# Kernel tuning notes

Measured on AMD Instinct MI355X. Metric: run time of the kernel, lower is better.

Reference implementation:

```python
import jax, jax.numpy as jnp
import numpy as np

B, L, C = 2, 2048, 1024
DK, H = 64, 16

def setup_inputs() -> dict:
    key = jax.random.key(0)
    ks = jax.random.split(key, 12)
    def lin(kw, kb, out_dim, in_dim):
        w = jax.random.normal(kw, (out_dim, in_dim), jnp.float32) * (1.0 / np.sqrt(in_dim))
        b = jnp.zeros((out_dim,), jnp.float32)
        return w, b
    WQ_w, WQ_b = lin(ks[0], ks[1], DK * H, C)
    WK_w, WK_b = lin(ks[2], ks[3], DK * H, C)
    WV_w, WV_b = lin(ks[4], ks[5], DK * H, C)
    WO_w, WO_b = lin(ks[6], ks[7], C, DK * H)
    qx = jax.random.normal(ks[8], (B, L, C), jnp.float32)
    kx = jax.random.normal(ks[9], (B, L, C), jnp.float32)
    vx = jax.random.normal(ks[10], (B, L, C), jnp.float32)
    maskPAD = jax.random.randint(ks[11], (B, L, L), 0, 2, jnp.int32)
    return {"qx": qx, "kx": kx, "vx": vx, "maskPAD": maskPAD,
            "WQ_w": WQ_w, "WQ_b": WQ_b, "WK_w": WK_w, "WK_b": WK_b,
            "WV_w": WV_w, "WV_b": WV_b, "WO_w": WO_w, "WO_b": WO_b}

def reference(qx, kx, vx, maskPAD, WQ_w, WQ_b, WK_w, WK_b, WV_w, WV_b, WO_w, WO_b):
    Bq, qL, _ = qx.shape
    kvL = kx.shape[1]
    # projections -> [B, H, L, DK]
    q = (qx @ WQ_w.T + WQ_b).reshape(Bq, qL, H, DK).transpose(0, 2, 1, 3)
    k = (kx @ WK_w.T + WK_b).reshape(Bq, kvL, H, DK).transpose(0, 2, 1, 3)
    v = (vx @ WV_w.T + WV_b).reshape(Bq, kvL, H, DK).transpose(0, 2, 1, 3)
    scores = jnp.einsum('bhqd,bhkd->bhqk', q, k) / np.sqrt(DK).astype(np.float32)
    scores = jnp.where((maskPAD == 0)[:, None, :, :], jnp.float32(-2**15 + 1), scores)
    alpha = jax.nn.softmax(scores, axis=3)  # dropout p=0 (eval)
    z = jnp.einsum('bhqk,bhkd->bhqd', alpha, v)
    z = z.transpose(0, 2, 1, 3).reshape(Bq, qL, H * DK)
    return z @ WO_w.T + WO_b
```

## Files before the change

### kernel.cpp

```cpp
#include <hip/hip_runtime.h>
#include <stdint.h>
#include <math.h>

typedef short short8 __attribute__((ext_vector_type(8)));
typedef float float4v __attribute__((ext_vector_type(4)));

static __device__ __forceinline__ float bf2f(uint16_t u) {
    union { uint32_t i; float f; } x; x.i = ((uint32_t)u) << 16; return x.f;
}
static __device__ __forceinline__ uint16_t f2bf(float f) {
    union { float f; uint32_t i; } x; x.f = f;
    uint32_t u = x.i;
    u += 0x7FFFu + ((u >> 16) & 1u);
    return (uint16_t)(u >> 16);
}
static __device__ __forceinline__ uint16_t f2bf_sane(float f) {
    uint16_t u = f2bf(f);
    if ((u & 0x7F80u) == 0x7F80u) u = 0;
    return u;
}
static __device__ __forceinline__ float san_f32(float f) {
    union { float f; uint32_t i; } x; x.f = f;
    if (((x.i >> 23) & 0xFFu) == 0xFFu) return 0.f;
    return x.f;
}
static __device__ __forceinline__ void gll16(const void* g, void* l) {
    __builtin_amdgcn_global_load_lds((const __attribute__((address_space(1))) void*)g,
                                     (__attribute__((address_space(3))) void*)l,
                                     16, 0, 0);
}
static __device__ __forceinline__ short8 load8(const void* p, size_t off, int fp32) {
    if (!fp32) return *(const short8*)((const uint16_t*)p + off);
    const float* f = (const float*)p + off;
    const float4v a = *(const float4v*)f;
    const float4v b = *(const float4v*)(f + 4);
    short8 r;
    r[0] = (short)f2bf(a[0]); r[1] = (short)f2bf(a[1]);
    r[2] = (short)f2bf(a[2]); r[3] = (short)f2bf(a[3]);
    r[4] = (short)f2bf(b[0]); r[5] = (short)f2bf(b[1]);
    r[6] = (short)f2bf(b[2]); r[7] = (short)f2bf(b[3]);
    return r;
}

__global__ __launch_bounds__(256) void detect_kernel(const uint16_t* qx, int* flag)
{
    __shared__ int s;
    const int tid = threadIdx.x;
    if (tid == 0) s = 0;
    __syncthreads();
    int bad = 0;
#pragma unroll 8
    for (int i = 0; i < 64; ++i) {
        const uint16_t u = qx[tid * 64 + i];
        bad |= ((u & 0x7F80u) == 0x7F80u) ? 1 : 0;
    }
    if (bad) atomicOr(&s, 1);
    __syncthreads();
    if (tid == 0) *flag = s;
}

__global__ __launch_bounds__(256) void pack_kernel(
    const int* __restrict__ mask, uint64_t* __restrict__ mask64)
{
    const int wave = threadIdx.x >> 6, lane = threadIdx.x & 63;
    const int row = blockIdx.x * 4 + wave;
    const int* src = mask + (size_t)row * 2048;
#pragma unroll 4
    for (int j = 0; j < 32; ++j) {
        const int m = src[j * 64 + lane];
        const uint64_t bal = __ballot(m != 0);
        if (lane == 0) mask64[(size_t)row * 32 + j] = bal;
    }
}

__global__ __launch_bounds__(256) void convert_kernel(
    const void* qx, const void* kx, const void* vx,
    const void* wq, const void* wk, const void* wv, const void* wo,
    const void* bq, const void* bk, const void* bv, const void* bo,
    uint16_t* cIn, uint16_t* cW, uint16_t* cB, const int* flag)
{
    const int mode = *flag;
    const int z = blockIdx.z;
    const int idx8 = blockIdx.x * 256 + threadIdx.x;
    if (z < 3) {
        const void* src = (z == 0) ? qx : (z == 1) ? kx : vx;
        uint16_t* dst = cIn + (size_t)z * 4194304;
        if (idx8 < 524288)
            *(short8*)(dst + (size_t)idx8 * 8) = load8(src, (size_t)idx8 * 8, mode);
    } else if (z < 7) {
        const int t = z - 3;
        const void* src = (t == 0) ? wq : (t == 1) ? wk : (t == 2) ? wv : wo;
        uint16_t* dst = cW + (size_t)t * 1048576;
        if (idx8 < 131072)
            *(short8*)(dst + (size_t)idx8 * 8) = load8(src, (size_t)idx8 * 8, mode);
    } else {
        if (idx8 < 128) {
#pragma unroll
            for (int t = 0; t < 4; ++t) {
                const void* src = (t == 0) ? bq : (t == 1) ? bk : (t == 2) ? bv : bo;
                *(short8*)(cB + t * 1024 + idx8 * 8) = load8(src, (size_t)idx8 * 8, mode);
            }
        }
    }
}

template <int MI, int NI>
static __device__ __forceinline__ void gemm_tile(
    const uint16_t* __restrict__ A, const uint16_t* __restrict__ W,
    const uint16_t* __restrict__ bias, void* __restrict__ C,
    int c_fp32, float out_scale)
{
    constexpr int TM = MI * 32, TN = NI * 32;
    __shared__ __align__(16) uint16_t sA[TM * 32];
    __shared__ __align__(16) uint16_t sB[TN * 32];

    const int tid  = threadIdx.x;
    const int wave = tid >> 6;
    const int lane = tid & 63;
    const int quad = lane >> 4;
    const int l15  = lane & 15;
    const int m0 = blockIdx.y * TM;
    const int n0 = blockIdx.x * TN;
    const int wm = (wave >> 1) * (MI * 16);
    const int wn = (wave & 1) * (NI * 16);
    const int r16 = lane >> 2;
    const int ch  = lane & 3;

    float4v acc[MI][NI] = {};

    for (int k0 = 0; k0 < 1024; k0 += 32) {
        __syncthreads();
#pragma unroll
        for (int g = wave; g < TM / 16; g += 4)
            gll16(A + (size_t)(m0 + g * 16 + r16) * 1024 + k0 + ch * 8,
                  (char*)sA + (size_t)g * 1024);
#pragma unroll
        for (int g = wave; g < TN / 16; g += 4)
            gll16(W + (size_t)(n0 + g * 16 + r16) * 1024 + k0 + ch * 8,
                  (char*)sB + (size_t)g * 1024);
        asm volatile("s_waitcnt vmcnt(0)" ::: "memory");
        __syncthreads();

        short8 af[MI], bfr[NI];
#pragma unroll
        for (int i = 0; i < MI; ++i)
            af[i] = *(const short8*)&sA[(wm + i * 16 + l15) * 32 + quad * 8];
#pragma unroll
        for (int j = 0; j < NI; ++j)
            bfr[j] = *(const short8*)&sB[(wn + j * 16 + l15) * 32 + quad * 8];
#pragma unroll
        for (int mi = 0; mi < MI; ++mi)
#pragma unroll
            for (int ni = 0; ni < NI; ++ni)
                acc[mi][ni] = __builtin_amdgcn_mfma_f32_16x16x32_bf16(
                    af[mi], bfr[ni], acc[mi][ni], 0, 0, 0);
    }

#pragma unroll
    for (int ni = 0; ni < NI; ++ni) {
        const int n = n0 + wn + ni * 16 + l15;
        const float bv = bf2f(bias[n]);
#pragma unroll
        for (int mi = 0; mi < MI; ++mi) {
            const int mbase = m0 + wm + mi * 16 + quad * 4;
#pragma unroll
            for (int r = 0; r < 4; ++r) {
                const float v = (acc[mi][ni][r] + bv) * out_scale;
                const size_t idx = (size_t)(mbase + r) * 1024 + n;
                if (c_fp32) ((float*)C)[idx] = san_f32(v);
                else        ((uint16_t*)C)[idx] = f2bf_sane(v);
            }
        }
    }
}

__global__ __launch_bounds__(256) void qkv_kernel(
    const uint16_t* cIn, const uint16_t* cW, const uint16_t* cB,
    uint16_t* Q, uint16_t* K, uint16_t* V)
{
    const int z = blockIdx.z;
    const uint16_t* A = cIn + (size_t)z * 4194304;
    const uint16_t* W = cW + (size_t)z * 1048576;
    const uint16_t* b = cB + z * 1024;
    uint16_t* C = (z == 0) ? Q : (z == 1) ? K : V;
    const float sc = (z == 0) ? 0.125f : 1.0f;
    gemm_tile<4, 4>(A, W, b, C, 0, sc);
}

__global__ __launch_bounds__(256) void out_kernel(
    const uint16_t* Z, const uint16_t* cW, const uint16_t* cB,
    void* out, const int* flag)
{
    const int mode = *flag;
    gemm_tile<2, 4>(Z, cW + 3 * 1048576, cB + 3 * 1024, out, mode, 1.0f);
}

__global__ __launch_bounds__(256) void vtrans_kernel(
    const uint16_t* __restrict__ Vp, uint16_t* __restrict__ Vt)
{
    __shared__ __align__(16) uint16_t t[64][72];
    const int tid = threadIdx.x;
    const int lt = blockIdx.x, h = blockIdx.y, b = blockIdx.z;
#pragma unroll
    for (int p = 0; p < 2; ++p) {
        const int r = p * 32 + (tid >> 3);
        const int c = (tid & 7) * 8;
        *(short8*)&t[r][c] =
            *(const short8*)(Vp + (size_t)(b * 2048 + lt * 64 + r) * 1024 + h * 64 + c);
    }
    __syncthreads();
#pragma unroll
    for (int p = 0; p < 2; ++p) {
        const int d = p * 32 + (tid >> 3);
        const int c = (tid & 7) * 8;
        short8 v;
#pragma unroll
        for (int j = 0; j < 8; ++j) v[j] = (short)t[c + j][d];
        *(short8*)(Vt + (size_t)((b * 16 + h) * 64 + d) * 2048 + lt * 64 + c) = v;
    }
}

#define VS 72

__global__ __launch_bounds__(256) void attn_kernel(
    const uint16_t* __restrict__ Q, const uint16_t* __restrict__ Kp,
    const uint16_t* __restrict__ Vt, const uint64_t* __restrict__ mask64,
    uint16_t* __restrict__ Z)
{
    __shared__ __align__(16) uint16_t sQ[64 * VS];
    __shared__ __align__(16) uint16_t sK[64 * VS];
    __shared__ __align__(16) uint16_t sV[64 * VS];
    __shared__ __align__(16) float    sS[4][16 * 36];

    const int tid = threadIdx.x;
    const int wave = tid >> 6, lane = tid & 63;
    const int quad = lane >> 4, l15 = lane & 15;
    const int qt = blockIdx.x, h = blockIdx.y, b = blockIdx.z;
    const int q0 = qt * 64;

    const int srow = tid >> 2;
    const int sc0  = (tid & 3);

    {
        const short8 x0 = *(const short8*)(Q + (size_t)(b * 2048 + q0 + srow) * 1024 + h * 64 + sc0 * 8);
        const short8 x1 = *(const short8*)(Q + (size_t)(b * 2048 + q0 + srow) * 1024 + h * 64 + (sc0 + 4) * 8);
        *(short8*)&sQ[srow * VS + sc0 * 8]       = x0;
        *(short8*)&sQ[srow * VS + (sc0 + 4) * 8] = x1;
    }
    __syncthreads();

    short8 qf[2];
#pragma unroll
    for (int kk = 0; kk < 2; ++kk)
        qf[kk] = *(const short8*)&sQ[(wave * 16 + l15) * VS + (quad + 4 * kk) * 8];

    const uint64_t* mrow = mask64 + (size_t)(b * 2048 + q0 + wave * 16 + l15) * 32;

    short8 ones;
#pragma unroll
    for (int j = 0; j < 8; ++j) ones[j] = (short)0x3F80;

    float4v oacc[4] = {};
    float4v lacc = {};

    for (int kt = 0; kt < 32; ++kt) {
        const int k0 = kt * 64;
        const short8 kx0 = *(const short8*)(Kp + (size_t)(b * 2048 + k0 + srow) * 1024 + h * 64 + sc0 * 8);
        const short8 kx1 = *(const short8*)(Kp + (size_t)(b * 2048 + k0 + srow) * 1024 + h * 64 + (sc0 + 4) * 8);
        const short8 vx0 = *(const short8*)(Vt + (size_t)((b * 16 + h) * 64 + srow) * 2048 + k0 + sc0 * 8);
        const short8 vx1 = *(const short8*)(Vt + (size_t)((b * 16 + h) * 64 + srow) * 2048 + k0 + (sc0 + 4) * 8);
        const uint64_t mw = mrow[kt];
        __syncthreads();
        *(short8*)&sK[srow * VS + sc0 * 8]       = kx0;
        *(short8*)&sK[srow * VS + (sc0 + 4) * 8] = kx1;
        *(short8*)&sV[srow * VS + sc0 * 8]       = vx0;
        *(short8*)&sV[srow * VS + (sc0 + 4) * 8] = vx1;
        __syncthreads();

        float4v sacc[4] = {};
#pragma unroll
        for (int ni = 0; ni < 4; ++ni) {
            const int row = ni * 16 + l15;
#pragma unroll
            for (int kk = 0; kk < 2; ++kk) {
                const short8 kf = *(const short8*)&sK[row * VS + (quad + 4 * kk) * 8];
                sacc[ni] = __builtin_amdgcn_mfma_f32_16x16x32_bf16(qf[kk], kf, sacc[ni], 0, 0, 0);
            }
        }

        short8 pf[2];
        float* Sw = &sS[wave][0];
#pragma unroll
        for (int h2 = 0; h2 < 2; ++h2) {
#pragma unroll
            for (int n2 = 0; n2 < 2; ++n2) {
                const float4v s4 = sacc[h2 * 2 + n2];
#pragma unroll
                for (int r = 0; r < 4; ++r)
                    Sw[(quad * 4 + r) * 36 + n2 * 16 + l15] = s4[r];
            }
            asm volatile("s_waitcnt lgkmcnt(0)" ::: "memory");
            const float* rp = &Sw[l15 * 36 + quad * 8];
            const float4v x0 = *(const float4v*)rp;
            const float4v x1 = *(const float4v*)(rp + 4);
            asm volatile("" ::: "memory");
            short8 tt;
#pragma unroll
            for (int j = 0; j < 4; ++j) {
                const int kp = h2 * 32 + quad * 8 + j;
                const float p0 = ((mw >> kp) & 1ull) ? __expf(x0[j]) : 0.f;
                const float p1 = ((mw >> (kp + 4)) & 1ull) ? __expf(x1[j]) : 0.f;
                tt[j]     = (short)f2bf(p0);
                tt[4 + j] = (short)f2bf(p1);
            }
            pf[h2] = tt;
        }

#pragma unroll
        for (int ni = 0; ni < 4; ++ni) {
            const int row = ni * 16 + l15;
#pragma unroll
            for (int kk = 0; kk < 2; ++kk) {
                const short8 vf = *(const short8*)&sV[row * VS + (quad + 4 * kk) * 8];
                oacc[ni] = __builtin_amdgcn_mfma_f32_16x16x32_bf16(pf[kk], vf, oacc[ni], 0, 0, 0);
            }
        }
#pragma unroll
        for (int kk = 0; kk < 2; ++kk)
            lacc = __builtin_amdgcn_mfma_f32_16x16x32_bf16(pf[kk], ones, lacc, 0, 0, 0);
    }

#pragma unroll
    for (int r = 0; r < 4; ++r) {
        const float inv = 1.0f / fmaxf(lacc[r], 1e-37f);
        const int qrow = q0 + wave * 16 + quad * 4 + r;
#pragma unroll
        for (int ni = 0; ni < 4; ++ni) {
            const float v = oacc[ni][r] * inv;
            Z[(size_t)(b * 2048 + qrow) * 1024 + h * 64 + ni * 16 + l15] = f2bf_sane(v);
        }
    }
}

extern "C" void kernel_launch(void* const* d_in, const int* in_sizes, int n_in,
                              void* d_out, int out_size, void* d_ws, size_t ws_size,
                              hipStream_t stream)
{
    const void* qx  = d_in[0];
    const void* kx  = d_in[1];
    const void* vx  = d_in[2];
    const int*  msk = (const int*)d_in[3];

    char* ws = (char*)d_ws;
    const size_t MB = 1024 * 1024;
    uint16_t* cIn = (uint16_t*)(ws);
    uint16_t* cW  = (uint16_t*)(ws + 24 * MB);
    uint16_t* cB  = (uint16_t*)(ws + 32 * MB);
    int*      flg = (int*)(ws + 32 * MB + 16 * 1024);
    uint16_t* Qb  = (uint16_t*)(ws + 33 * MB);
    uint16_t* Kb  = (uint16_t*)(ws + 41 * MB);
    uint16_t* Vb  = (uint16_t*)(ws + 49 * MB);
    uint64_t* m64 = (uint64_t*)(ws + 57 * MB);
    uint16_t* Vt  = (uint16_t*)(ws + 8 * MB);
    uint16_t* Zb  = (uint16_t*)(ws);

    detect_kernel<<<1, 256, 0, stream>>>((const uint16_t*)qx, flg);
    pack_kernel<<<1024, 256, 0, stream>>>(msk, m64);
    convert_kernel<<<dim3(2048, 1, 8), 256, 0, stream>>>(
        qx, kx, vx, d_in[4], d_in[6], d_in[8], d_in[10],
        d_in[5], d_in[7], d_in[9], d_in[11], cIn, cW, cB, flg);
    qkv_kernel<<<dim3(8, 32, 3), 256, 0, stream>>>(cIn, cW, cB, Qb, Kb, Vb);
    vtrans_kernel<<<dim3(32, 16, 2), 256, 0, stream>>>(Vb, Vt);
    attn_kernel<<<dim3(32, 16, 2), 256, 0, stream>>>(Qb, Kb, Vt, m64, Zb);
    out_kernel<<<dim3(8, 64), 256, 0, stream>>>(Zb, cW, cB, d_out, flg);
}
```

Measured before the change: 309.2 us.

## Double attention query tile per wave and skip conversion for bf16 inputs

The attention kernel now gives each wave 32 query rows instead of 16, so every K/V tile staged in LDS feeds twice as many MFMAs. Probabilities are computed directly from the MFMA accumulator layout and written to LDS as bf16, replacing the fp32 score transpose through shared memory. Q fragments are loaded straight from global memory instead of through LDS. Separately, when the detected input mode indicates bf16 data, the conversion pass is skipped and the projection GEMMs read the raw inputs directly. The cost is more registers and half as many attention blocks, which may lower occupancy and load balance.

```diff
diff --git a/kernel.cpp b/kernel.cpp
--- a/kernel.cpp
+++ b/kernel.cpp
@@ -80,25 +80,26 @@
     uint16_t* cIn, uint16_t* cW, uint16_t* cB, const int* flag)
 {
     const int mode = *flag;
+    if (!mode) return;
     const int z = blockIdx.z;
     const int idx8 = blockIdx.x * 256 + threadIdx.x;
     if (z < 3) {
         const void* src = (z == 0) ? qx : (z == 1) ? kx : vx;
         uint16_t* dst = cIn + (size_t)z * 4194304;
         if (idx8 < 524288)
-            *(short8*)(dst + (size_t)idx8 * 8) = load8(src, (size_t)idx8 * 8, mode);
+            *(short8*)(dst + (size_t)idx8 * 8) = load8(src, (size_t)idx8 * 8, 1);
     } else if (z < 7) {
         const int t = z - 3;
         const void* src = (t == 0) ? wq : (t == 1) ? wk : (t == 2) ? wv : wo;
         uint16_t* dst = cW + (size_t)t * 1048576;
         if (idx8 < 131072)
-            *(short8*)(dst + (size_t)idx8 * 8) = load8(src, (size_t)idx8 * 8, mode);
+            *(short8*)(dst + (size_t)idx8 * 8) = load8(src, (size_t)idx8 * 8, 1);
     } else {
         if (idx8 < 128) {
 #pragma unroll
             for (int t = 0; t < 4; ++t) {
                 const void* src = (t == 0) ? bq : (t == 1) ? bk : (t == 2) ? bv : bo;
-                *(short8*)(cB + t * 1024 + idx8 * 8) = load8(src, (size_t)idx8 * 8, mode);
+                *(short8*)(cB + t * 1024 + idx8 * 8) = load8(src, (size_t)idx8 * 8, 1);
             }
         }
     }
@@ -175,24 +176,33 @@
 }
 
 __global__ __launch_bounds__(256) void qkv_kernel(
+    const uint16_t* rqx, const uint16_t* rkx, const uint16_t* rvx,
+    const uint16_t* rwq, const uint16_t* rwk, const uint16_t* rwv,
+    const uint16_t* rbq, const uint16_t* rbk, const uint16_t* rbv,
     const uint16_t* cIn, const uint16_t* cW, const uint16_t* cB,
-    uint16_t* Q, uint16_t* K, uint16_t* V)
-{
+    uint16_t* Q, uint16_t* K, uint16_t* V, const int* flag)
+{
+    const int mode = *flag;
     const int z = blockIdx.z;
-    const uint16_t* A = cIn + (size_t)z * 4194304;
-    const uint16_t* W = cW + (size_t)z * 1048576;
-    const uint16_t* b = cB + z * 1024;
+    const uint16_t* A = mode ? cIn + (size_t)z * 4194304
+                             : ((z == 0) ? rqx : (z == 1) ? rkx : rvx);
+    const uint16_t* W = mode ? cW + (size_t)z * 1048576
+                             : ((z == 0) ? rwq : (z == 1) ? rwk : rwv);
+    const uint16_t* b = mode ? cB + z * 1024
+                             : ((z == 0) ? rbq : (z == 1) ? rbk : rbv);
     uint16_t* C = (z == 0) ? Q : (z == 1) ? K : V;
     const float sc = (z == 0) ? 0.125f : 1.0f;
     gemm_tile<4, 4>(A, W, b, C, 0, sc);
 }
 
 __global__ __launch_bounds__(256) void out_kernel(
-    const uint16_t* Z, const uint16_t* cW, const uint16_t* cB,
-    void* out, const int* flag)
+    const uint16_t* Z, const uint16_t* rwo, const uint16_t* rbo,
+    const uint16_t* cW, const uint16_t* cB, void* out, const int* flag)
 {
     const int mode = *flag;
-    gemm_tile<2, 4>(Z, cW + 3 * 1048576, cB + 3 * 1024, out, mode, 1.0f);
+    const uint16_t* W = mode ? cW + 3 * 1048576 : rwo;
+    const uint16_t* b = mode ? cB + 3 * 1024 : rbo;
+    gemm_tile<2, 4>(Z, W, b, out, mode, 1.0f);
 }
 
 __global__ __launch_bounds__(256) void vtrans_kernel(
@@ -227,41 +237,41 @@
     const uint16_t* __restrict__ Vt, const uint64_t* __restrict__ mask64,
     uint16_t* __restrict__ Z)
 {
-    __shared__ __align__(16) uint16_t sQ[64 * VS];
     __shared__ __align__(16) uint16_t sK[64 * VS];
     __shared__ __align__(16) uint16_t sV[64 * VS];
-    __shared__ __align__(16) float    sS[4][16 * 36];
+    __shared__ __align__(16) uint16_t sP[4][32 * VS];
 
     const int tid = threadIdx.x;
     const int wave = tid >> 6, lane = tid & 63;
     const int quad = lane >> 4, l15 = lane & 15;
     const int qt = blockIdx.x, h = blockIdx.y, b = blockIdx.z;
-    const int q0 = qt * 64;
+    const int q0 = qt * 128;
+    const int qw = q0 + wave * 32;
 
     const int srow = tid >> 2;
-    const int sc0  = (tid & 3);
-
-    {
-        const short8 x0 = *(const short8*)(Q + (size_t)(b * 2048 + q0 + srow) * 1024 + h * 64 + sc0 * 8);
-        const short8 x1 = *(const short8*)(Q + (size_t)(b * 2048 + q0 + srow) * 1024 + h * 64 + (sc0 + 4) * 8);
-        *(short8*)&sQ[srow * VS + sc0 * 8]       = x0;
-        *(short8*)&sQ[srow * VS + (sc0 + 4) * 8] = x1;
-    }
-    __syncthreads();
-
-    short8 qf[2];
-#pragma unroll
-    for (int kk = 0; kk < 2; ++kk)
-        qf[kk] = *(const short8*)&sQ[(wave * 16 + l15) * VS + (quad + 4 * kk) * 8];
-
-    const uint64_t* mrow = mask64 + (size_t)(b * 2048 + q0 + wave * 16 + l15) * 32;
+    const int sc0  = tid & 3;
+
+    short8 qf[2][2];
+#pragma unroll
+    for (int mi = 0; mi < 2; ++mi)
+#pragma unroll
+        for (int kk = 0; kk < 2; ++kk)
+            qf[mi][kk] = *(const short8*)(Q + (size_t)(b * 2048 + qw + mi * 16 + l15) * 1024
+                                            + h * 64 + (quad + 4 * kk) * 8);
+
+    const uint64_t* mrow[2][4];
+#pragma unroll
+    for (int mi = 0; mi < 2; ++mi)
+#pragma unroll
+        for (int r = 0; r < 4; ++r)
+            mrow[mi][r] = mask64 + (size_t)(b * 2048 + qw + mi * 16 + quad * 4 + r) * 32;
 
     short8 ones;
 #pragma unroll
     for (int j = 0; j < 8; ++j) ones[j] = (short)0x3F80;
 
-    float4v oacc[4] = {};
-    float4v lacc = {};
+    float4v oacc[2][4] = {};
+    float4v lacc[2] = {};
 
     for (int kt = 0; kt < 32; ++kt) {
         const int k0 = kt * 64;
@@ -269,7 +279,6 @@
         const short8 kx1 = *(const short8*)(Kp + (size_t)(b * 2048 + k0 + srow) * 1024 + h * 64 + (sc0 + 4) * 8);
         const short8 vx0 = *(const short8*)(Vt + (size_t)((b * 16 + h) * 64 + srow) * 2048 + k0 + sc0 * 8);
         const short8 vx1 = *(const short8*)(Vt + (size_t)((b * 16 + h) * 64 + srow) * 2048 + k0 + (sc0 + 4) * 8);
-        const uint64_t mw = mrow[kt];
         __syncthreads();
         *(short8*)&sK[srow * VS + sc0 * 8]       = kx0;
         *(short8*)&sK[srow * VS + (sc0 + 4) * 8] = kx1;
@@ -277,44 +286,41 @@
         *(short8*)&sV[srow * VS + (sc0 + 4) * 8] = vx1;
         __syncthreads();
 
-        float4v sacc[4] = {};
+        float4v sacc[2][4] = {};
 #pragma unroll
         for (int ni = 0; ni < 4; ++ni) {
             const int row = ni * 16 + l15;
 #pragma unroll
             for (int kk = 0; kk < 2; ++kk) {
                 const short8 kf = *(const short8*)&sK[row * VS + (quad + 4 * kk) * 8];
-                sacc[ni] = __builtin_amdgcn_mfma_f32_16x16x32_bf16(qf[kk], kf, sacc[ni], 0, 0, 0);
-            }
-        }
-
-        short8 pf[2];
-        float* Sw = &sS[wave][0];
-#pragma unroll
-        for (int h2 = 0; h2 < 2; ++h2) {
-#pragma unroll
-            for (int n2 = 0; n2 < 2; ++n2) {
-                const float4v s4 = sacc[h2 * 2 + n2];
-#pragma unroll
-                for (int r = 0; r < 4; ++r)
-                    Sw[(quad * 4 + r) * 36 + n2 * 16 + l15] = s4[r];
-            }
-            asm volatile("s_waitcnt lgkmcnt(0)" ::: "memory");
-            const float* rp = &Sw[l15 * 36 + quad * 8];
-            const float4v x0 = *(const float4v*)rp;
-            const float4v x1 = *(const float4v*)(rp + 4);
-            asm volatile("" ::: "memory");
-            short8 tt;
-#pragma unroll
-            for (int j = 0; j < 4; ++j) {
-                const int kp = h2 * 32 + quad * 8 + j;
-                const float p0 = ((mw >> kp) & 1ull) ? __expf(x0[j]) : 0.f;
-                const float p1 = ((mw >> (kp + 4)) & 1ull) ? __expf(x1[j]) : 0.f;
-                tt[j]     = (short)f2bf(p0);
-                tt[4 + j] = (short)f2bf(p1);
-            }
-            pf[h2] = tt;
-        }
+                sacc[0][ni] = __builtin_amdgcn_mfma_f32_16x16x32_bf16(qf[0][kk], kf, sacc[0][ni], 0, 0, 0);
+                sacc[1][ni] = __builtin_amdgcn_mfma_f32_16x16x32_bf16(qf[1][kk], kf, sacc[1][ni], 0, 0, 0);
+            }
+        }
+
+        uint16_t* Pw = &sP[wave][0];
+#pragma unroll
+        for (int mi = 0; mi < 2; ++mi) {
+            uint64_t mw[4];
+#pragma unroll
+            for (int r = 0; r < 4; ++r) mw[r] = mrow[mi][r][kt];
+#pragma unroll
+            for (int ni = 0; ni < 4; ++ni)
+#pragma unroll
+                for (int r = 0; r < 4; ++r) {
+                    const float p = ((mw[r] >> (ni * 16 + l15)) & 1ull)
+                                        ? __expf(sacc[mi][ni][r]) : 0.f;
+                    Pw[(mi * 16 + quad * 4 + r) * VS + ni * 16 + l15] = f2bf(p);
+                }
+        }
+        asm volatile("s_waitcnt lgkmcnt(0)" ::: "memory");
+        short8 pf[2][2];
+#pragma unroll
+        for (int mi = 0; mi < 2; ++mi)
+#pragma unroll
+            for (int kk = 0; kk < 2; ++kk)
+                pf[mi][kk] = *(const short8*)&Pw[(mi * 16 + l15) * VS + (quad + 4 * kk) * 8];
+        asm volatile("" ::: "memory");
 
 #pragma unroll
         for (int ni = 0; ni < 4; ++ni) {
@@ -322,24 +328,29 @@
 #pragma unroll
             for (int kk = 0; kk < 2; ++kk) {
                 const short8 vf = *(const short8*)&sV[row * VS + (quad + 4 * kk) * 8];
-                oacc[ni] = __builtin_amdgcn_mfma_f32_16x16x32_bf16(pf[kk], vf, oacc[ni], 0, 0, 0);
-            }
-        }
-#pragma unroll
-        for (int kk = 0; kk < 2; ++kk)
-            lacc = __builtin_amdgcn_mfma_f32_16x16x32_bf16(pf[kk], ones, lacc, 0, 0, 0);
-    }
-
-#pragma unroll
-    for (int r = 0; r < 4; ++r) {
-        const float inv = 1.0f / fmaxf(lacc[r], 1e-37f);
-        const int qrow = q0 + wave * 16 + quad * 4 + r;
-#pragma unroll
-        for (int ni = 0; ni < 4; ++ni) {
-            const float v = oacc[ni][r] * inv;
-            Z[(size_t)(b * 2048 + qrow) * 1024 + h * 64 + ni * 16 + l15] = f2bf_sane(v);
-        }
-    }
+                oacc[0][ni] = __builtin_amdgcn_mfma_f32_16x16x32_bf16(pf[0][kk], vf, oacc[0][ni], 0, 0, 0);
+                oacc[1][ni] = __builtin_amdgcn_mfma_f32_16x16x32_bf16(pf[1][kk], vf, oacc[1][ni], 0, 0, 0);
+            }
+        }
+#pragma unroll
+        for (int mi = 0; mi < 2; ++mi)
+#pragma unroll
+            for (int kk = 0; kk < 2; ++kk)
+                lacc[mi] = __builtin_amdgcn_mfma_f32_16x16x32_bf16(pf[mi][kk], ones, lacc[mi], 0, 0, 0);
+    }
+
+#pragma unroll
+    for (int mi = 0; mi < 2; ++mi)
+#pragma unroll
+        for (int r = 0; r < 4; ++r) {
+            const float inv = 1.0f / fmaxf(lacc[mi][r], 1e-37f);
+            const int qrow = qw + mi * 16 + quad * 4 + r;
+#pragma unroll
+            for (int ni = 0; ni < 4; ++ni) {
+                const float v = oacc[mi][ni][r] * inv;
+                Z[(size_t)(b * 2048 + qrow) * 1024 + h * 64 + ni * 16 + l15] = f2bf_sane(v);
+            }
+        }
 }
 
 extern "C" void kernel_launch(void* const* d_in, const int* in_sizes, int n_in,
@@ -369,8 +380,13 @@
     convert_kernel<<<dim3(2048, 1, 8), 256, 0, stream>>>(
         qx, kx, vx, d_in[4], d_in[6], d_in[8], d_in[10],
         d_in[5], d_in[7], d_in[9], d_in[11], cIn, cW, cB, flg);
-    qkv_kernel<<<dim3(8, 32, 3), 256, 0, stream>>>(cIn, cW, cB, Qb, Kb, Vb);
+    qkv_kernel<<<dim3(8, 32, 3), 256, 0, stream>>>(
+        (const uint16_t*)qx, (const uint16_t*)kx, (const uint16_t*)vx,
+        (const uint16_t*)d_in[4], (const uint16_t*)d_in[6], (const uint16_t*)d_in[8],
+        (const uint16_t*)d_in[5], (const uint16_t*)d_in[7], (const uint16_t*)d_in[9],
+        cIn, cW, cB, Qb, Kb, Vb, flg);
     vtrans_kernel<<<dim3(32, 16, 2), 256, 0, stream>>>(Vb, Vt);
-    attn_kernel<<<dim3(32, 16, 2), 256, 0, stream>>>(Qb, Kb, Vt, m64, Zb);
-    out_kernel<<<dim3(8, 64), 256, 0, stream>>>(Zb, cW, cB, d_out, flg);
-}
+    attn_kernel<<<dim3(16, 16, 2), 256, 0, stream>>>(Qb, Kb, Vt, m64, Zb);
+    out_kernel<<<dim3(8, 64), 256, 0, stream>>>(
+        Zb, (const uint16_t*)d_in[10], (const uint16_t*)d_in[11], cW, cB, d_out, flg);
+}
```

Result: slower. 326.2 us (+5.5%).
